# Optimization experiments

Hardware: AMD Instinct MI355X
Metric: run time of the kernel (lower is better)

Reference implementation:

```python
import jax, jax.numpy as jnp
import numpy as np

MAX_SPAN_WIDTH = 12
THRESHOLD = 0.5


def _span_table(num_words):
    starts, ends = [], []
    for s in range(num_words):
        for e in range(s, min(num_words, s + MAX_SPAN_WIDTH)):
            starts.append(s)
            ends.append(e)
    return np.asarray(starts, np.int32), np.asarray(ends, np.int32)


def _mlp(x, w1, b1, w2, b2):
    # Linear -> LeakyReLU(0.01) -> Linear
    return jax.nn.leaky_relu(x @ w1 + b1, negative_slope=0.01) @ w2 + b2


def setup_inputs() -> dict:
    B, L, H, E, W, DFF = 8, 1024, 768, 16, 504, 512
    key = jax.random.key(0)
    ks = jax.random.split(key, 9)
    hidden_states = jax.random.normal(ks[0], (B, L, H), dtype=jnp.float32)
    # layout: first E tokens are entity-type tokens, next 2*W tokens are text (2 subwords/word)
    ent_mask = np.zeros((B, L), np.int32); ent_mask[:, :E] = 1
    text_mask = np.zeros((B, L), np.int32); text_mask[:, E:E + 2 * W] = 1
    word_index = np.full((B, L), -1, np.int32)
    word_index[:, E:E + 2 * W] = np.repeat(np.arange(W, dtype=np.int32), 2)[None, :]
    s = 0.02
    return {
        "hidden_states": hidden_states,
        "ent_w1": jax.random.normal(ks[1], (H, DFF), jnp.float32) * s,
        "ent_b1": jnp.zeros((DFF,), jnp.float32),
        "ent_w2": jax.random.normal(ks[2], (DFF, H), jnp.float32) * s,
        "ent_b2": jnp.zeros((H,), jnp.float32),
        "span_w1": jax.random.normal(ks[3], (2 * H, DFF), jnp.float32) * s,
        "span_b1": jnp.zeros((DFF,), jnp.float32),
        "span_w2": jax.random.normal(ks[4], (DFF, H), jnp.float32) * s,
        "span_b2": jnp.zeros((H,), jnp.float32),
        "text_mask": jnp.asarray(text_mask),
        "ent_mask": jnp.asarray(ent_mask),
        "word_index": jnp.asarray(word_index),
        "num_words": W,
        "num_ent": E,
    }


def reference(hidden_states, ent_w1, ent_b1, ent_w2, ent_b2,
              span_w1, span_b1, span_w2, span_b2,
              text_mask, ent_mask, word_index, num_words, num_ent):
    B, L, H = hidden_states.shape
    W, E = int(num_words), int(num_ent)

    # ---- word-level mean pooling over subword tokens (WordTokenRepresentation) ----
    valid = (text_mask == 1) & (word_index >= 0)                       # [B,L]
    oh = ((word_index[..., None] == jnp.arange(W)) & valid[..., None]).astype(hidden_states.dtype)  # [B,L,W]
    counts = jnp.maximum(oh.sum(axis=1), 1.0)                          # [B,W]
    word_emb = jnp.einsum('blw,blh->bwh', oh, hidden_states) / counts[..., None]

    # ---- gather entity-type tokens in order (EntityTokenRepresentation) ----
    keyv = jnp.where(ent_mask == 1, jnp.arange(L), L + jnp.arange(L))
    ent_pos = jnp.argsort(keyv, axis=-1)[:, :E]                        # [B,E]
    ent_tok = jnp.take_along_axis(hidden_states, ent_pos[..., None], axis=1)  # [B,E,H]
    ent_vec = _mlp(ent_tok, ent_w1, ent_b1, ent_w2, ent_b2)            # [B,E,H]

    # ---- span representations (all spans of width < MAX_SPAN_WIDTH) ----
    starts_np, ends_np = _span_table(W)                                # [N]
    span_in = jnp.concatenate([word_emb[:, starts_np], word_emb[:, ends_np]], axis=-1)  # [B,N,2H]
    span_vec = _mlp(span_in, span_w1, span_b1, span_w2, span_b2)       # [B,N,H]

    # ---- matching logits ----
    logits = jnp.einsum('bnh,beh->bne', span_vec, ent_vec)             # [B,N,E]

    # ---- NMS-style greedy decode (flat mode): threshold + score sort + overlap rejection ----
    N = logits.shape[1]
    probs = jax.nn.sigmoid(logits).reshape(B, N * E)
    cstart = jnp.repeat(jnp.asarray(starts_np), E)                     # [N*E]
    cend = jnp.repeat(jnp.asarray(ends_np), E)
    order = jnp.argsort(-probs, axis=-1)                               # score-descending
    probs_s = jnp.take_along_axis(probs, order, axis=-1)
    s_s, e_s = cstart[order], cend[order]
    pos = jnp.arange(W)

    def decode_one(pr, ss, ee):
        def body(cov, x):
            p, s, e = x
            m = (pos >= s) & (pos <= e)                                # candidate span mask over words
            take = (p > THRESHOLD) & ~jnp.any(cov & m)                 # flat: reject any overlap
            return cov | (m & take), take
        _, taken = jax.lax.scan(body, jnp.zeros((W,), bool), (pr, ss, ee))
        return taken

    taken_sorted = jax.vmap(decode_one)(probs_s, s_s, e_s)             # [B,N*E]
    inv = jnp.argsort(order, axis=-1)
    selected = jnp.take_along_axis(taken_sorted, inv, axis=-1).reshape(B, N, E)
    return logits, selected
```

## Files before the change

kernel.cpp:

```cpp
#include <hip/hip_runtime.h>
#include <hip/hip_bf16.h>
#include <stdint.h>

#define B_ 8
#define L_ 1024
#define H_ 768
#define E_ 16
#define W_ 504
#define DFF_ 512
#define N_ 5982
#define NE_ (N_*E_)
#define BNE_ (B_*NE_)
#define MAXK48 0x0000FFFFFFFFFFFFull
#define PT_ 24

typedef unsigned long long u64;
typedef unsigned int u32;

__device__ __forceinline__ int rowstart_of(int s){
    int s0 = W_ - 11;
    if (s <= s0) return 12*s;
    int t = s - s0;
    return 12*s0 + t*11 - (t*(t-1))/2;
}

__global__ void k_prolog(const int* __restrict__ ent_mask, int* __restrict__ ent_pos,
                         int* __restrict__ starts, int* __restrict__ ends,
                         int* __restrict__ tokc){
    int blk = blockIdx.x; int tid = threadIdx.x;
    if (blk == 8){
        for (int s = tid; s < W_; s += 256){
            int rs = rowstart_of(s);
            int cnt = min(12, W_ - s);
            for (int i = 0; i < cnt; i++){ starts[rs+i] = s; ends[rs+i] = s+i; }
        }
        for (int i = tid; i < B_*W_; i += 256) tokc[i] = 0;
        return;
    }
    __shared__ u32 wt[4]; __shared__ u32 cbase;
    int b = blk;
    int lane = tid & 63, wave = tid >> 6;
    if (tid == 0) cbase = 0;
    __syncthreads();
    for (int base = 0; base < L_; base += 256){
        int l = base + tid;
        bool f = (ent_mask[b*L_ + l] == 1);
        u64 bal = __ballot(f);
        if (lane == 0) wt[wave] = (u32)__popcll(bal);
        __syncthreads();
        u32 pre = cbase;
        for (int w = 0; w < 4; w++) if (w < wave) pre += wt[w];
        if (f){
            u32 rank = pre + (u32)__popcll(bal & ((1ull<<lane)-1ull));
            if (rank < E_) ent_pos[b*E_ + rank] = l;
        }
        __syncthreads();
        if (tid == 0){ u32 r = cbase; for (int w = 0; w < 4; w++) r += wt[w]; cbase = r; }
        __syncthreads();
    }
    u32 totEnt = cbase;
    if (totEnt >= E_) return;
    for (int base = 0; base < L_; base += 256){
        int l = base + tid;
        bool f = (ent_mask[b*L_ + l] != 1);
        u64 bal = __ballot(f);
        if (lane == 0) wt[wave] = (u32)__popcll(bal);
        __syncthreads();
        u32 pre = cbase;
        for (int w = 0; w < 4; w++) if (w < wave) pre += wt[w];
        if (f){
            u32 rank = pre + (u32)__popcll(bal & ((1ull<<lane)-1ull));
            if (rank < E_) ent_pos[b*E_ + rank] = l;
        }
        __syncthreads();
        if (tid == 0){ u32 r = cbase; for (int w = 0; w < 4; w++) r += wt[w]; cbase = r; }
        __syncthreads();
    }
}

__global__ void k_toklist(const int* __restrict__ tm, const int* __restrict__ wi,
                          int* __restrict__ tok, int* __restrict__ tokc){
    int i = blockIdx.x*256 + threadIdx.x;
    if (i >= B_*L_) return;
    int w = wi[i];
    if (tm[i] == 1 && w >= 0 && w < W_){
        int b = i / L_;
        int bw = b*W_ + w;
        int pos = atomicAdd(&tokc[bw], 1);
        if (pos < 4) tok[bw*4 + pos] = i - b*L_;
    }
}

__global__ void k_poolsort(const float* __restrict__ hs, const int* __restrict__ tok,
                           const int* __restrict__ tokc, float* __restrict__ wemb){
    __shared__ int stok[4]; __shared__ int scnt;
    int bw = blockIdx.x;
    int b = bw / W_;
    int tid = threadIdx.x;
    if (tid == 0){
        int c = tokc[bw]; int cc = min(c, 4);
        int v[4];
        for (int k = 0; k < cc; k++) v[k] = tok[bw*4 + k];
        for (int a = 1; a < cc; a++){ int x = v[a]; int j = a-1; while (j >= 0 && v[j] > x){ v[j+1] = v[j]; j--; } v[j+1] = x; }
        for (int k = 0; k < cc; k++) stok[k] = v[k];
        scnt = c;
    }
    __syncthreads();
    int c = scnt; int cc = min(c, 4);
    float denom = (float)max(c, 1);
    for (int h = tid; h < H_; h += 256){
        double s = 0.0;
        for (int k = 0; k < cc; k++)
            s += (double)hs[((size_t)(b*L_ + stok[k]))*H_ + h];
        wemb[(size_t)bw*H_ + h] = (float)(s / (double)denom);
    }
}

__global__ void k_ent(const float* __restrict__ hs, const int* __restrict__ ent_pos,
                      const float* __restrict__ w1, const float* __restrict__ b1,
                      const float* __restrict__ w2, const float* __restrict__ b2,
                      float* __restrict__ ent_vec){
    __shared__ float x[H_];
    __shared__ float hid[DFF_];
    int be = blockIdx.x;
    int b = be >> 4;
    int tid = threadIdx.x;
    int pos = ent_pos[be];
    const float* xp = hs + ((size_t)b*L_ + pos)*H_;
    for (int j = tid; j < H_; j += 256) x[j] = xp[j];
    __syncthreads();
    #pragma unroll
    for (int q = 0; q < 2; q++){
        int d = q*256 + tid;
        float a0=0.f,a1=0.f,a2=0.f,a3=0.f;
        const float* wp = w1 + d;
        #pragma unroll 4
        for (int h = 0; h < H_; h += 4){
            a0 += x[h+0]*wp[(size_t)(h+0)*DFF_];
            a1 += x[h+1]*wp[(size_t)(h+1)*DFF_];
            a2 += x[h+2]*wp[(size_t)(h+2)*DFF_];
            a3 += x[h+3]*wp[(size_t)(h+3)*DFF_];
        }
        float acc = ((a0+a1)+(a2+a3)) + b1[d];
        hid[d] = acc > 0.f ? acc : 0.01f*acc;
    }
    __syncthreads();
    #pragma unroll
    for (int q = 0; q < 3; q++){
        int j = q*256 + tid;
        float a0=0.f,a1=0.f,a2=0.f,a3=0.f;
        const float* wp = w2 + j;
        #pragma unroll 4
        for (int d = 0; d < DFF_; d += 4){
            a0 += hid[d+0]*wp[(size_t)(d+0)*H_];
            a1 += hid[d+1]*wp[(size_t)(d+1)*H_];
            a2 += hid[d+2]*wp[(size_t)(d+2)*H_];
            a3 += hid[d+3]*wp[(size_t)(d+3)*H_];
        }
        ent_vec[(size_t)be*H_ + j] = ((a0+a1)+(a2+a3)) + b2[j];
    }
}

__global__ void k_Mc(const float* __restrict__ span_w2, const float* __restrict__ span_b2,
                     const float* __restrict__ ent_vec, float* __restrict__ M,
                     float* __restrict__ cvec){
    int blk = blockIdx.x;
    if (blk == 256){
        int i = threadIdx.x;
        if (i < B_*E_){
            const float* ev = ent_vec + (size_t)i*H_;
            double acc = 0.0;
            for (int h = 0; h < H_; h++) acc += (double)span_b2[h]*(double)ev[h];
            cvec[i] = (float)acc;
        }
        return;
    }
    int b = blk/32; int dbase = (blk%32)*16;
    int tid = threadIdx.x; int d = dbase + (tid>>4); int e = tid&15;
    const float* ev = ent_vec + ((size_t)b*E_ + e)*H_;
    const float* wr = span_w2 + (size_t)d*H_;
    double p0=0.0, p1=0.0;
    for (int h = 0; h < H_; h += 2){
        p0 += (double)wr[h]*(double)ev[h];
        p1 += (double)wr[h+1]*(double)ev[h+1];
    }
    M[((size_t)b*DFF_ + d)*E_ + e] = (float)(p0+p1);
}

__global__ void k_pq(const float* __restrict__ wemb, const float* __restrict__ w1,
                     float* __restrict__ PQ, int b0){
    __shared__ float As[16][68];
    __shared__ float Bs[16][68];
    int bx = blockIdx.x & 15;
    int by = blockIdx.x >> 4;
    int tid = threadIdx.x;
    int tm = tid >> 4, tn = tid & 15;
    const float* A0 = wemb + (size_t)b0*W_*H_;
    int colbase = bx*64;
    const float* Bbase = (colbase < DFF_) ? w1 : (w1 + (size_t)H_*DFF_);
    int bcol0 = (colbase < DFF_) ? colbase : (colbase - DFF_);
    float acc[4][4] = {{0.f}};
    int ar = tid >> 2, akq = tid & 3;
    int bkk = tid >> 4, bcq = tid & 15;
    const int ROWS = 4*W_;
    for (int k0 = 0; k0 < H_; k0 += 16){
        {
            int gr = by*64 + ar;
            float4 av;
            if (gr < ROWS) av = *(const float4*)(A0 + (size_t)gr*H_ + k0 + akq*4);
            else av = make_float4(0.f,0.f,0.f,0.f);
            As[akq*4+0][ar] = av.x; As[akq*4+1][ar] = av.y;
            As[akq*4+2][ar] = av.z; As[akq*4+3][ar] = av.w;
        }
        {
            float4 bv = *(const float4*)(Bbase + (size_t)(k0+bkk)*DFF_ + bcol0 + bcq*4);
            Bs[bkk][bcq*4+0] = bv.x; Bs[bkk][bcq*4+1] = bv.y;
            Bs[bkk][bcq*4+2] = bv.z; Bs[bkk][bcq*4+3] = bv.w;
        }
        __syncthreads();
        #pragma unroll
        for (int kk = 0; kk < 16; kk++){
            float4 a = *(const float4*)&As[kk][tm*4];
            float4 bv = *(const float4*)&Bs[kk][tn*4];
            acc[0][0] += a.x*bv.x; acc[0][1] += a.x*bv.y; acc[0][2] += a.x*bv.z; acc[0][3] += a.x*bv.w;
            acc[1][0] += a.y*bv.x; acc[1][1] += a.y*bv.y; acc[1][2] += a.y*bv.z; acc[1][3] += a.y*bv.w;
            acc[2][0] += a.z*bv.x; acc[2][1] += a.z*bv.y; acc[2][2] += a.z*bv.z; acc[2][3] += a.z*bv.w;
            acc[3][0] += a.w*bv.x; acc[3][1] += a.w*bv.y; acc[3][2] += a.w*bv.z; acc[3][3] += a.w*bv.w;
        }
        __syncthreads();
    }
    #pragma unroll
    for (int r = 0; r < 4; r++){
        int gr = by*64 + tm*4 + r;
        if (gr < ROWS){
            float4 ov = make_float4(acc[r][0], acc[r][1], acc[r][2], acc[r][3]);
            *(float4*)(PQ + (size_t)gr*1024 + colbase + tn*4) = ov;
        }
    }
}

__global__ void k_logits(const float* __restrict__ PQ, const float* __restrict__ Mmat,
                         const float* __restrict__ cvec, const float* __restrict__ span_b1,
                         float* __restrict__ logits, float* __restrict__ outL, int b0){
    __shared__ float Ps[DFF_];
    __shared__ float hid[DFF_];
    __shared__ double redw[64];
    __shared__ float csh[E_];
    int blk = blockIdx.x;
    int bl = blk / W_; int s = blk - bl*W_;
    int b = b0 + bl;
    int tid = threadIdx.x;
    int lane = tid & 63, wave = tid >> 6;
    int ee = tid & 15; int g = tid >> 4;
    float Mreg[32];
    {
        const float* Mp = Mmat + (size_t)b*DFF_*E_ + (size_t)(g*32)*E_ + ee;
        #pragma unroll
        for (int i = 0; i < 32; i++) Mreg[i] = Mp[(size_t)i*E_];
    }
    const float* P = PQ + ((size_t)(bl*W_ + s))*1024;
    for (int d = tid; d < DFF_; d += 256) Ps[d] = P[d] + span_b1[d];
    if (tid < E_) csh[tid] = cvec[b*E_ + tid];
    __syncthreads();
    int nsp = min(12, W_ - s);
    int nbase = rowstart_of(s);
    for (int i = 0; i < nsp; i++){
        int e = s + i;
        const float* Q = PQ + ((size_t)(bl*W_ + e))*1024 + DFF_;
        for (int d = tid; d < DFF_; d += 256){
            float h = Ps[d] + Q[d];
            hid[d] = h > 0.f ? h : 0.01f*h;
        }
        __syncthreads();
        {
            double acc = 0.0;
            int d0 = g*32;
            #pragma unroll
            for (int k = 0; k < 32; k++) acc += (double)hid[d0+k]*(double)Mreg[k];
            double t = acc + __shfl_down(acc, 32, 64);
            t = t + __shfl_down(t, 16, 64);
            if (lane < 16) redw[wave*16 + lane] = t;
        }
        __syncthreads();
        if (tid < E_){
            double t = ((redw[tid] + redw[16+tid]) + (redw[32+tid] + redw[48+tid]))
                     + (double)csh[tid];
            float lg = (float)t;
            size_t oi = ((size_t)b*N_ + nbase + i)*E_ + tid;
            logits[oi] = lg;
            outL[oi] = lg;
        }
        __syncthreads();
    }
}

__global__ void k_spanbest(const float* __restrict__ logits,
                           const int* __restrict__ starts, const int* __restrict__ ends,
                           u64* __restrict__ candS, float* __restrict__ outSel){
    int idx = blockIdx.x*256 + threadIdx.x;
    if (idx >= B_*N_) return;
    int b = idx / N_; int n = idx - b*N_;
    const float* lg = logits + (size_t)b*NE_ + (size_t)n*16;
    u64 best = ~0ull;
    for (int e = 0; e < 16; e++){
        float prob = 1.0f/(1.0f + expf(-lg[e]));
        if (prob > 0.5f){
            u32 key24 = (~__float_as_uint(prob)) & 0xFFFFFFu;
            u64 pk = ((u64)key24 << 24) | (u64)(u32)(n*16 + e);
            best = best < pk ? best : pk;
        }
    }
    int s = starts[n], e2 = ends[n];
    int len = e2 - s + 1;
    u64 packed = best;
    if (best != ~0ull)
        packed = best | ((u64)(u32)s << 48) | ((u64)(u32)(len-1) << 57);
    candS[idx] = packed;
    float* selp = outSel + (size_t)BNE_ + (size_t)b*NE_ + (size_t)n*16;
    float4 z = make_float4(0.f,0.f,0.f,0.f);
    *(float4*)(selp+0)  = z; *(float4*)(selp+4)  = z;
    *(float4*)(selp+8)  = z; *(float4*)(selp+12) = z;
}

__device__ __forceinline__ void decode_wave(const u64* sp, int n,
                                            float* __restrict__ outSel, int b){
    int lane = threadIdx.x & 63;
    u64 scov[8];
    #pragma unroll
    for (int k = 0; k < 8; k++) scov[k] = 0ull;
    int covcnt = 0;
    for (int base = 0; base < n; base += 64){
        int i = base + lane;
        bool has = i < n;
        u64 v = has ? sp[i] : ~0ull;
        int s   = (int)((v >> 48) & 0x1FFull);
        int len = (int)((v >> 57) & 0xFull) + 1;
        u32 c   = (u32)(v & 0xFFFFFFull);
        int w0 = s >> 6, sh0 = s & 63;
        int w1i = (w0 < 7) ? w0 + 1 : 7;
        u64 full = (1ull << len) - 1ull;
        u64 m0 = has ? (full << sh0) : 0ull;
        u64 m1 = (has && sh0 + len > 64) ? (full >> (64 - sh0)) : 0ull;
        u64 myc0 = 0ull, myc1 = 0ull;
        #pragma unroll
        for (int k = 0; k < 8; k++){
            if (w0  == k) myc0 = scov[k];
            if (w1i == k) myc1 = scov[k];
        }
        bool tent = has && (((myc0 & m0) | (myc1 & m1)) == 0ull);
        u64 bal = __ballot(tent);
        u32 vlo = (u32)v, vhi = (u32)(v >> 32);
        u64 acc = 0ull;
        while (bal){
            int j = (int)__builtin_ctzll(bal);
            bal &= bal - 1ull;
#if __has_builtin(__builtin_amdgcn_readlane)
            u32 jlo = (u32)__builtin_amdgcn_readlane((int)vlo, j);
            u32 jhi = (u32)__builtin_amdgcn_readlane((int)vhi, j);
#else
            u32 jlo = (u32)__shfl((int)vlo, j, 64);
            u32 jhi = (u32)__shfl((int)vhi, j, 64);
#endif
            u64 jv = ((u64)jhi << 32) | (u64)jlo;
            int js   = (int)((jv >> 48) & 0x1FFull);
            int jlen = (int)((jv >> 57) & 0xFull) + 1;
            int jw0 = js >> 6, jsh = js & 63;
            int jw1 = (jw0 < 7) ? jw0 + 1 : 7;
            u64 jfull = (1ull << jlen) - 1ull;
            u64 jm0 = jfull << jsh;
            u64 jm1 = (jsh + jlen > 64) ? (jfull >> (64 - jsh)) : 0ull;
            u64 c0 = 0ull, c1 = 0ull;
            #pragma unroll
            for (int k = 0; k < 8; k++){
                if (jw0 == k) c0 = scov[k];
                if (jw1 == k) c1 = scov[k];
            }
            bool ok = (((c0 & jm0) | (c1 & jm1)) == 0ull);
            u64 okm = ok ? ~0ull : 0ull;
            #pragma unroll
            for (int k = 0; k < 8; k++){
                u64 add = 0ull;
                if (jw0 == k) add |= jm0;
                if (jw1 == k) add |= jm1;
                scov[k] |= (add & okm);
            }
            covcnt += ok ? jlen : 0;
            acc |= (okm & (1ull << j));
        }
        if (((acc >> lane) & 1ull) != 0ull)
            outSel[(size_t)BNE_ + (size_t)b*NE_ + (size_t)c] = 1.0f;
        if (covcnt >= W_) break;
    }
}

__global__ __launch_bounds__(256) void k_tail(const u64* __restrict__ candS,
                                              float* __restrict__ outSel){
    __shared__ u64 cs[6032];
    __shared__ u64 Ma[512], Mb[512];
    __shared__ u32 wtot[4];
    __shared__ int nsh;
    int b = blockIdx.x; int tid = threadIdx.x;
    int lane = tid & 63, wave = tid >> 6;
    const u64* cSg = candS + (size_t)b*N_;

    for (int i = tid; i < N_; i += 256) cs[i] = cSg[i];
    __syncthreads();

    for (int s = tid; s < 512; s += 256)
        Ma[s] = (s < W_) ? (cs[rowstart_of(s)] & MAXK48) : MAXK48;
    __syncthreads();
    u64* Mcur = Ma; u64* Mnext = Mb;
    for (int l = 2; l <= 12; l++){
        #pragma unroll
        for (int q = 0; q < 2; q++){
            int s = tid + q*256;
            u64 key = MAXK48; int idx = -1;
            if (s + l <= W_){ idx = rowstart_of(s) + (l-1); key = cs[idx] & MAXK48; }
            u64 a = Mcur[s];
            u64 bb = (s + 1 < 512) ? Mcur[s+1] : MAXK48;
            u64 dom = a < bb ? a : bb;
            if (idx >= 0 && dom < key) cs[idx] = ~0ull;
            Mnext[s] = dom < key ? dom : key;
        }
        __syncthreads();
        u64* t = Mcur; Mcur = Mnext; Mnext = t;
    }

    {
        int base = tid*PT_;
        u64 vv[PT_];
        u32 flags = 0; int cnt = 0;
        #pragma unroll
        for (int k = 0; k < PT_; k++){
            int i = base + k;
            u64 v = (i < N_) ? cs[i] : ~0ull;
            vv[k] = v;
            if (v != ~0ull){ flags |= (1u << k); cnt++; }
        }
        u32 inc = (u32)cnt;
        for (int d = 1; d < 64; d <<= 1){ u32 o = (u32)__shfl_up((int)inc, d, 64); if (lane >= d) inc += o; }
        if (lane == 63) wtot[wave] = inc;
        __syncthreads();
        u32 woffs = 0;
        for (int w = 0; w < 4; w++) if (w < wave) woffs += wtot[w];
        u32 off = woffs + inc - (u32)cnt;
        if (tid == 255) nsh = (int)(woffs + inc);
        #pragma unroll
        for (int k = 0; k < PT_; k++){
            if (flags & (1u << k)) cs[off++] = vv[k];
        }
    }
    __syncthreads();
    int n = nsh;
    if (tid < 8) cs[n + tid] = ~0ull;
    __syncthreads();

    if (n <= 1024){
        u64 v0=~0ull, v1=~0ull, v2=~0ull, v3=~0ull;
        u64 k0=0, k1=0, k2=0, k3=0;
        if (tid       < n){ v0 = cs[tid];       k0 = v0 & MAXK48; }
        if (tid + 256 < n){ v1 = cs[tid + 256]; k1 = v1 & MAXK48; }
        if (tid + 512 < n){ v2 = cs[tid + 512]; k2 = v2 & MAXK48; }
        if (tid + 768 < n){ v3 = cs[tid + 768]; k3 = v3 & MAXK48; }
        u32 r0=0, r1=0, r2=0, r3=0;
        for (int j = 0; j < n; j += 8){
            u64 c0 = cs[j+0] & MAXK48, c1 = cs[j+1] & MAXK48;
            u64 c2 = cs[j+2] & MAXK48, c3 = cs[j+3] & MAXK48;
            u64 c4 = cs[j+4] & MAXK48, c5 = cs[j+5] & MAXK48;
            u64 c6 = cs[j+6] & MAXK48, c7 = cs[j+7] & MAXK48;
            r0 += (u32)(c0<k0) + (u32)(c1<k0) + (u32)(c2<k0) + (u32)(c3<k0)
                + (u32)(c4<k0) + (u32)(c5<k0) + (u32)(c6<k0) + (u32)(c7<k0);
            r1 += (u32)(c0<k1) + (u32)(c1<k1) + (u32)(c2<k1) + (u32)(c3<k1)
                + (u32)(c4<k1) + (u32)(c5<k1) + (u32)(c6<k1) + (u32)(c7<k1);
            r2 += (u32)(c0<k2) + (u32)(c1<k2) + (u32)(c2<k2) + (u32)(c3<k2)
                + (u32)(c4<k2) + (u32)(c5<k2) + (u32)(c6<k2) + (u32)(c7<k2);
            r3 += (u32)(c0<k3) + (u32)(c1<k3) + (u32)(c2<k3) + (u32)(c3<k3)
                + (u32)(c4<k3) + (u32)(c5<k3) + (u32)(c6<k3) + (u32)(c7<k3);
        }
        __syncthreads();
        if (tid       < n) cs[r0] = v0;
        if (tid + 256 < n) cs[r1] = v1;
        if (tid + 512 < n) cs[r2] = v2;
        if (tid + 768 < n) cs[r3] = v3;
        __syncthreads();
    } else {
        u64 vv[PT_]; u32 rr[PT_];
        #pragma unroll
        for (int k = 0; k < PT_; k++){ vv[k] = ~0ull; rr[k] = 0; }
        #pragma unroll
        for (int k = 0; k < PT_; k++){
            int i = tid + (k << 8);
            if (i < n){
                u64 v = cs[i];
                vv[k] = v;
                u64 ki = v & MAXK48;
                u32 r = 0;
                for (int j = 0; j < n; j += 8){
                    u64 c0 = cs[j+0]&MAXK48, c1 = cs[j+1]&MAXK48;
                    u64 c2 = cs[j+2]&MAXK48, c3 = cs[j+3]&MAXK48;
                    u64 c4 = cs[j+4]&MAXK48, c5 = cs[j+5]&MAXK48;
                    u64 c6 = cs[j+6]&MAXK48, c7 = cs[j+7]&MAXK48;
                    r += (u32)(c0<ki) + (u32)(c1<ki) + (u32)(c2<ki) + (u32)(c3<ki)
                       + (u32)(c4<ki) + (u32)(c5<ki) + (u32)(c6<ki) + (u32)(c7<ki);
                }
                rr[k] = r;
            }
        }
        __syncthreads();
        #pragma unroll
        for (int k = 0; k < PT_; k++){
            int i = tid + (k << 8);
            if (i < n) cs[rr[k]] = vv[k];
        }
        __syncthreads();
    }

    if (wave == 0) decode_wave(cs, n, outSel, b);
}

extern "C" void kernel_launch(void* const* d_in, const int* in_sizes, int n_in,
                              void* d_out, int out_size, void* d_ws, size_t ws_size,
                              hipStream_t stream){
    const float* hs        = (const float*)d_in[0];
    const float* ent_w1    = (const float*)d_in[1];
    const float* ent_b1    = (const float*)d_in[2];
    const float* ent_w2    = (const float*)d_in[3];
    const float* ent_b2    = (const float*)d_in[4];
    const float* span_w1   = (const float*)d_in[5];
    const float* span_b1   = (const float*)d_in[6];
    const float* span_w2   = (const float*)d_in[7];
    const float* span_b2   = (const float*)d_in[8];
    const int*  text_mask  = (const int*)d_in[9];
    const int*  ent_mask   = (const int*)d_in[10];
    const int*  word_index = (const int*)d_in[11];
    float* out = (float*)d_out;

    char* wsbase = (char*)d_ws; size_t off = 0;
    auto alloc = [&](size_t bytes)->void*{ void* p = wsbase + off; off = (off + bytes + 255) & ~(size_t)255; return p; };
    char*  region1 = (char*)alloc((size_t)B_*W_*H_*4);
    float* wemb   = (float*)region1;
    u64*   candS  = (u64*)region1;
    int*   tok    = (int*)  alloc((size_t)B_*W_*4*4);
    int*   tokc   = (int*)  alloc((size_t)B_*W_*4);
    float* PQ     = (float*)alloc((size_t)4*W_*1024*4);
    float* logits = (float*)alloc((size_t)BNE_*4);
    int*   entpos = (int*)  alloc((size_t)B_*E_*4);
    float* entvec = (float*)alloc((size_t)B_*E_*H_*4);
    float* Mmat   = (float*)alloc((size_t)B_*DFF_*E_*4);
    float* cvec   = (float*)alloc((size_t)B_*E_*4);
    int*   starts = (int*)  alloc((size_t)N_*4);
    int*   ends   = (int*)  alloc((size_t)N_*4);

    k_prolog<<<9,256,0,stream>>>(ent_mask, entpos, starts, ends, tokc);
    k_toklist<<<(B_*L_+255)/256,256,0,stream>>>(text_mask, word_index, tok, tokc);
    k_poolsort<<<B_*W_,256,0,stream>>>(hs, tok, tokc, wemb);
    k_ent<<<B_*E_,256,0,stream>>>(hs, entpos, ent_w1, ent_b1, ent_w2, ent_b2, entvec);
    k_Mc<<<257,256,0,stream>>>(span_w2, span_b2, entvec, Mmat, cvec);
    for (int b0 = 0; b0 < B_; b0 += 4){
        k_pq<<<512,256,0,stream>>>(wemb, span_w1, PQ, b0);
        k_logits<<<4*W_,256,0,stream>>>(PQ, Mmat, cvec, span_b1, logits, out, b0);
    }
    k_spanbest<<<(B_*N_+255)/256,256,0,stream>>>(logits, starts, ends, candS, out);
    k_tail<<<B_,256,0,stream>>>(candS, out);
}
```

Before: 512.4 us.

## Resolve greedy span conflicts with wave prefix-OR and widen tail rank sort

```diff
diff --git a/kernel.cpp b/kernel.cpp
--- a/kernel.cpp
+++ b/kernel.cpp
@@ -22,6 +22,17 @@
     if (s <= s0) return 12*s;
     int t = s - s0;
     return 12*s0 + t*11 - (t*(t-1))/2;
+}
+
+__device__ __forceinline__ u64 shflup_u64(u64 x, int d){
+    u32 lo = (u32)__shfl_up((int)(u32)x, d, 64);
+    u32 hi = (u32)__shfl_up((int)(u32)(x >> 32), d, 64);
+    return ((u64)hi << 32) | (u64)lo;
+}
+__device__ __forceinline__ u64 shflxor_u64(u64 x, int m){
+    u32 lo = (u32)__shfl_xor((int)(u32)x, m, 64);
+    u32 hi = (u32)__shfl_xor((int)(u32)(x >> 32), m, 64);
+    return ((u64)hi << 32) | (u64)lo;
 }
 
 __global__ void k_prolog(const int* __restrict__ ent_mask, int* __restrict__ ent_pos,
@@ -273,10 +284,16 @@
         }
         __syncthreads();
         {
-            double acc = 0.0;
             int d0 = g*32;
+            double a0=0.0, a1=0.0, a2=0.0, a3=0.0;
             #pragma unroll
-            for (int k = 0; k < 32; k++) acc += (double)hid[d0+k]*(double)Mreg[k];
+            for (int k = 0; k < 32; k += 4){
+                a0 += (double)hid[d0+k+0]*(double)Mreg[k+0];
+                a1 += (double)hid[d0+k+1]*(double)Mreg[k+1];
+                a2 += (double)hid[d0+k+2]*(double)Mreg[k+2];
+                a3 += (double)hid[d0+k+3]*(double)Mreg[k+3];
+            }
+            double acc = (a0+a1)+(a2+a3);
             double t = acc + __shfl_down(acc, 32, 64);
             t = t + __shfl_down(t, 16, 64);
             if (lane < 16) redw[wave*16 + lane] = t;
@@ -347,47 +364,98 @@
             if (w0  == k) myc0 = scov[k];
             if (w1i == k) myc1 = scov[k];
         }
-        bool tent = has && (((myc0 & m0) | (myc1 & m1)) == 0ull);
-        u64 bal = __ballot(tent);
-        u32 vlo = (u32)v, vhi = (u32)(v >> 32);
-        u64 acc = 0ull;
-        while (bal){
-            int j = (int)__builtin_ctzll(bal);
-            bal &= bal - 1ull;
-#if __has_builtin(__builtin_amdgcn_readlane)
-            u32 jlo = (u32)__builtin_amdgcn_readlane((int)vlo, j);
-            u32 jhi = (u32)__builtin_amdgcn_readlane((int)vhi, j);
-#else
-            u32 jlo = (u32)__shfl((int)vlo, j, 64);
-            u32 jhi = (u32)__shfl((int)vhi, j, 64);
-#endif
-            u64 jv = ((u64)jhi << 32) | (u64)jlo;
-            int js   = (int)((jv >> 48) & 0x1FFull);
-            int jlen = (int)((jv >> 57) & 0xFull) + 1;
-            int jw0 = js >> 6, jsh = js & 63;
-            int jw1 = (jw0 < 7) ? jw0 + 1 : 7;
-            u64 jfull = (1ull << jlen) - 1ull;
-            u64 jm0 = jfull << jsh;
-            u64 jm1 = (jsh + jlen > 64) ? (jfull >> (64 - jsh)) : 0ull;
-            u64 c0 = 0ull, c1 = 0ull;
+        bool alive = has && (((myc0 & m0) | (myc1 & m1)) == 0ull);
+        bool accept = false;
+        u64 balv = __ballot(alive);
+        if (balv){
+            u64 pm[8];
             #pragma unroll
             for (int k = 0; k < 8; k++){
-                if (jw0 == k) c0 = scov[k];
-                if (jw1 == k) c1 = scov[k];
-            }
-            bool ok = (((c0 & jm0) | (c1 & jm1)) == 0ull);
-            u64 okm = ok ? ~0ull : 0ull;
+                u64 t = 0ull;
+                if (alive){
+                    if (w0  == k) t |= m0;
+                    if (w1i == k) t |= m1;
+                }
+                pm[k] = t;
+            }
+            #pragma unroll
+            for (int st = 1; st < 64; st <<= 1){
+                #pragma unroll
+                for (int k = 0; k < 8; k++) pm[k] |= shflup_u64(pm[k], st);
+            }
+            u64 ex0 = 0ull, ex1 = 0ull;
             #pragma unroll
             for (int k = 0; k < 8; k++){
-                u64 add = 0ull;
-                if (jw0 == k) add |= jm0;
-                if (jw1 == k) add |= jm1;
-                scov[k] |= (add & okm);
-            }
-            covcnt += ok ? jlen : 0;
-            acc |= (okm & (1ull << j));
-        }
-        if (((acc >> lane) & 1ull) != 0ull)
+                u64 e = shflup_u64(pm[k], 1);
+                e = (lane == 0) ? 0ull : e;
+                if (w0  == k) ex0 = e;
+                if (w1i == k) ex1 = e;
+            }
+            bool blocked = (((ex0 & m0) | (ex1 & m1)) != 0ull);
+            bool newacc = alive && !blocked;
+            accept = newacc;
+            u64 am[8];
+            #pragma unroll
+            for (int k = 0; k < 8; k++){
+                u64 t = 0ull;
+                if (newacc){
+                    if (w0  == k) t |= m0;
+                    if (w1i == k) t |= m1;
+                }
+                am[k] = t;
+            }
+            #pragma unroll
+            for (int st = 1; st < 64; st <<= 1){
+                #pragma unroll
+                for (int k = 0; k < 8; k++) am[k] |= shflxor_u64(am[k], st);
+            }
+            #pragma unroll
+            for (int k = 0; k < 8; k++){
+                covcnt += (int)__popcll(am[k]);
+                scov[k] |= am[k];
+            }
+            u64 pend = __ballot(alive && blocked);
+            u32 vlo = (u32)v, vhi = (u32)(v >> 32);
+            u64 accm = 0ull;
+            while (pend){
+                int j = (int)__builtin_ctzll(pend);
+                pend &= pend - 1ull;
+#if __has_builtin(__builtin_amdgcn_readlane)
+                u32 jlo = (u32)__builtin_amdgcn_readlane((int)vlo, j);
+                u32 jhi = (u32)__builtin_amdgcn_readlane((int)vhi, j);
+#else
+                u32 jlo = (u32)__shfl((int)vlo, j, 64);
+                u32 jhi = (u32)__shfl((int)vhi, j, 64);
+#endif
+                u64 jv = ((u64)jhi << 32) | (u64)jlo;
+                int js   = (int)((jv >> 48) & 0x1FFull);
+                int jlen = (int)((jv >> 57) & 0xFull) + 1;
+                int jw0 = js >> 6, jsh = js & 63;
+                int jw1 = (jw0 < 7) ? jw0 + 1 : 7;
+                u64 jfull = (1ull << jlen) - 1ull;
+                u64 jm0 = jfull << jsh;
+                u64 jm1 = (jsh + jlen > 64) ? (jfull >> (64 - jsh)) : 0ull;
+                u64 c0 = 0ull, c1 = 0ull;
+                #pragma unroll
+                for (int k = 0; k < 8; k++){
+                    if (jw0 == k) c0 = scov[k];
+                    if (jw1 == k) c1 = scov[k];
+                }
+                bool ok = (((c0 & jm0) | (c1 & jm1)) == 0ull);
+                u64 okm = ok ? ~0ull : 0ull;
+                #pragma unroll
+                for (int k = 0; k < 8; k++){
+                    u64 add = 0ull;
+                    if (jw0 == k) add |= jm0;
+                    if (jw1 == k) add |= jm1;
+                    scov[k] |= (add & okm);
+                }
+                covcnt += ok ? jlen : 0;
+                accm |= (okm & (1ull << j));
+            }
+            if (((accm >> lane) & 1ull) != 0ull) accept = true;
+        }
+        if (accept)
             outSel[(size_t)BNE_ + (size_t)b*NE_ + (size_t)c] = 1.0f;
         if (covcnt >= W_) break;
     }
@@ -403,7 +471,9 @@
     int lane = tid & 63, wave = tid >> 6;
     const u64* cSg = candS + (size_t)b*N_;
 
-    for (int i = tid; i < N_; i += 256) cs[i] = cSg[i];
+    #pragma unroll
+    for (int k = 0; k < 23; k++) cs[tid + k*256] = cSg[tid + k*256];
+    { int i23 = tid + 23*256; if (i23 < N_) cs[i23] = cSg[i23]; }
     __syncthreads();
 
     for (int s = tid; s < 512; s += 256)
@@ -452,36 +522,44 @@
     }
     __syncthreads();
     int n = nsh;
-    if (tid < 8) cs[n + tid] = ~0ull;
-    __syncthreads();
-
-    if (n <= 1024){
-        u64 v0=~0ull, v1=~0ull, v2=~0ull, v3=~0ull;
-        u64 k0=0, k1=0, k2=0, k3=0;
-        if (tid       < n){ v0 = cs[tid];       k0 = v0 & MAXK48; }
-        if (tid + 256 < n){ v1 = cs[tid + 256]; k1 = v1 & MAXK48; }
-        if (tid + 512 < n){ v2 = cs[tid + 512]; k2 = v2 & MAXK48; }
-        if (tid + 768 < n){ v3 = cs[tid + 768]; k3 = v3 & MAXK48; }
-        u32 r0=0, r1=0, r2=0, r3=0;
-        for (int j = 0; j < n; j += 8){
-            u64 c0 = cs[j+0] & MAXK48, c1 = cs[j+1] & MAXK48;
-            u64 c2 = cs[j+2] & MAXK48, c3 = cs[j+3] & MAXK48;
-            u64 c4 = cs[j+4] & MAXK48, c5 = cs[j+5] & MAXK48;
-            u64 c6 = cs[j+6] & MAXK48, c7 = cs[j+7] & MAXK48;
-            r0 += (u32)(c0<k0) + (u32)(c1<k0) + (u32)(c2<k0) + (u32)(c3<k0)
-                + (u32)(c4<k0) + (u32)(c5<k0) + (u32)(c6<k0) + (u32)(c7<k0);
-            r1 += (u32)(c0<k1) + (u32)(c1<k1) + (u32)(c2<k1) + (u32)(c3<k1)
-                + (u32)(c4<k1) + (u32)(c5<k1) + (u32)(c6<k1) + (u32)(c7<k1);
-            r2 += (u32)(c0<k2) + (u32)(c1<k2) + (u32)(c2<k2) + (u32)(c3<k2)
-                + (u32)(c4<k2) + (u32)(c5<k2) + (u32)(c6<k2) + (u32)(c7<k2);
-            r3 += (u32)(c0<k3) + (u32)(c1<k3) + (u32)(c2<k3) + (u32)(c3<k3)
-                + (u32)(c4<k3) + (u32)(c5<k3) + (u32)(c6<k3) + (u32)(c7<k3);
-        }
-        __syncthreads();
-        if (tid       < n) cs[r0] = v0;
-        if (tid + 256 < n) cs[r1] = v1;
-        if (tid + 512 < n) cs[r2] = v2;
-        if (tid + 768 < n) cs[r3] = v3;
+    if (tid < 16) cs[n + tid] = ~0ull;
+    __syncthreads();
+
+    if (n <= 1536){
+        u64 v0=~0ull,v1=~0ull,v2=~0ull,v3=~0ull,v4=~0ull,v5=~0ull;
+        u64 k0=0,k1=0,k2=0,k3=0,k4=0,k5=0;
+        if (tid        < n){ v0 = cs[tid];        k0 = v0 & MAXK48; }
+        if (tid +  256 < n){ v1 = cs[tid +  256]; k1 = v1 & MAXK48; }
+        if (tid +  512 < n){ v2 = cs[tid +  512]; k2 = v2 & MAXK48; }
+        if (tid +  768 < n){ v3 = cs[tid +  768]; k3 = v3 & MAXK48; }
+        if (tid + 1024 < n){ v4 = cs[tid + 1024]; k4 = v4 & MAXK48; }
+        if (tid + 1280 < n){ v5 = cs[tid + 1280]; k5 = v5 & MAXK48; }
+        u32 r0=0,r1=0,r2=0,r3=0,r4=0,r5=0;
+        for (int j = 0; j < n; j += 16){
+            u64 c0 = cs[j+ 0]&MAXK48, c1 = cs[j+ 1]&MAXK48, c2 = cs[j+ 2]&MAXK48, c3 = cs[j+ 3]&MAXK48;
+            u64 c4 = cs[j+ 4]&MAXK48, c5 = cs[j+ 5]&MAXK48, c6 = cs[j+ 6]&MAXK48, c7 = cs[j+ 7]&MAXK48;
+            u64 c8 = cs[j+ 8]&MAXK48, c9 = cs[j+ 9]&MAXK48, cA = cs[j+10]&MAXK48, cB = cs[j+11]&MAXK48;
+            u64 cC = cs[j+12]&MAXK48, cD = cs[j+13]&MAXK48, cE = cs[j+14]&MAXK48, cF = cs[j+15]&MAXK48;
+            r0 += (u32)(c0<k0)+(u32)(c1<k0)+(u32)(c2<k0)+(u32)(c3<k0)+(u32)(c4<k0)+(u32)(c5<k0)+(u32)(c6<k0)+(u32)(c7<k0)
+                + (u32)(c8<k0)+(u32)(c9<k0)+(u32)(cA<k0)+(u32)(cB<k0)+(u32)(cC<k0)+(u32)(cD<k0)+(u32)(cE<k0)+(u32)(cF<k0);
+            r1 += (u32)(c0<k1)+(u32)(c1<k1)+(u32)(c2<k1)+(u32)(c3<k1)+(u32)(c4<k1)+(u32)(c5<k1)+(u32)(c6<k1)+(u32)(c7<k1)
+                + (u32)(c8<k1)+(u32)(c9<k1)+(u32)(cA<k1)+(u32)(cB<k1)+(u32)(cC<k1)+(u32)(cD<k1)+(u32)(cE<k1)+(u32)(cF<k1);
+            r2 += (u32)(c0<k2)+(u32)(c1<k2)+(u32)(c2<k2)+(u32)(c3<k2)+(u32)(c4<k2)+(u32)(c5<k2)+(u32)(c6<k2)+(u32)(c7<k2)
+                + (u32)(c8<k2)+(u32)(c9<k2)+(u32)(cA<k2)+(u32)(cB<k2)+(u32)(cC<k2)+(u32)(cD<k2)+(u32)(cE<k2)+(u32)(cF<k2);
+            r3 += (u32)(c0<k3)+(u32)(c1<k3)+(u32)(c2<k3)+(u32)(c3<k3)+(u32)(c4<k3)+(u32)(c5<k3)+(u32)(c6<k3)+(u32)(c7<k3)
+                + (u32)(c8<k3)+(u32)(c9<k3)+(u32)(cA<k3)+(u32)(cB<k3)+(u32)(cC<k3)+(u32)(cD<k3)+(u32)(cE<k3)+(u32)(cF<k3);
+            r4 += (u32)(c0<k4)+(u32)(c1<k4)+(u32)(c2<k4)+(u32)(c3<k4)+(u32)(c4<k4)+(u32)(c5<k4)+(u32)(c6<k4)+(u32)(c7<k4)
+                + (u32)(c8<k4)+(u32)(c9<k4)+(u32)(cA<k4)+(u32)(cB<k4)+(u32)(cC<k4)+(u32)(cD<k4)+(u32)(cE<k4)+(u32)(cF<k4);
+            r5 += (u32)(c0<k5)+(u32)(c1<k5)+(u32)(c2<k5)+(u32)(c3<k5)+(u32)(c4<k5)+(u32)(c5<k5)+(u32)(c6<k5)+(u32)(c7<k5)
+                + (u32)(c8<k5)+(u32)(c9<k5)+(u32)(cA<k5)+(u32)(cB<k5)+(u32)(cC<k5)+(u32)(cD<k5)+(u32)(cE<k5)+(u32)(cF<k5);
+        }
+        __syncthreads();
+        if (tid        < n) cs[r0] = v0;
+        if (tid +  256 < n) cs[r1] = v1;
+        if (tid +  512 < n) cs[r2] = v2;
+        if (tid +  768 < n) cs[r3] = v3;
+        if (tid + 1024 < n) cs[r4] = v4;
+        if (tid + 1280 < n) cs[r5] = v5;
         __syncthreads();
     } else {
         u64 vv[PT_]; u32 rr[PT_];
```

Result: faster. 487.6 us (-4.9%).
